# Kernel tuning notes

Hardware: AMD Instinct MI355X
Metric: run time of the kernel (lower is better)

## Reference

```python
import jax, jax.numpy as jnp
import numpy as np

INPUT_SIZE = 1024
HIDDEN_SIZE = 1024
B, L = 32, 2048


def setup_inputs() -> dict:
    key = jax.random.key(0)
    k_h, k_m, k_lw, k_vw, k_vq = jax.random.split(key, 5)
    h = jax.random.normal(k_h, (B, L, INPUT_SIZE), dtype=jnp.float32)
    mask = jax.random.randint(k_m, (B, L), 0, 2).astype(bool)
    # nn.Linear(input+hidden, hidden): weight (hidden, input+hidden), bias (hidden,)
    fan = INPUT_SIZE + HIDDEN_SIZE + HIDDEN_SIZE
    ln_w = jax.random.uniform(k_lw, (HIDDEN_SIZE, INPUT_SIZE + HIDDEN_SIZE),
                              minval=-1.0, maxval=1.0, dtype=jnp.float32) * np.sqrt(6.0 / fan)
    ln_b = jnp.zeros((HIDDEN_SIZE,), dtype=jnp.float32)
    # v: Linear(hidden, 1, bias=False) -> weight (1, hidden); store as (hidden,)
    v_w = jax.random.uniform(k_vw, (HIDDEN_SIZE,), minval=-1.0, maxval=1.0,
                             dtype=jnp.float32) * np.sqrt(6.0 / (HIDDEN_SIZE + 1))
    vq = jax.random.uniform(k_vq, (HIDDEN_SIZE,), dtype=jnp.float32)
    return {"h": h, "mask": mask, "ln_w": ln_w, "ln_b": ln_b, "v_w": v_w, "vq": vq}


def reference(h, mask, ln_w, ln_b, v_w, vq):
    # ln(cat([h, vq], -1)) == h @ W_h^T + vq @ W_vq^T + b  (vq is constant over b,l)
    W_h = ln_w[:, :INPUT_SIZE]          # (H, I)
    W_vq = ln_w[:, INPUT_SIZE:]         # (H, H)
    bias = ln_b + W_vq @ vq             # (H,)
    pre = jnp.einsum('bli,hi->blh', h, W_h) + bias  # (B, L, H)
    s = jnp.tanh(pre) @ v_w             # (B, L)
    s = s - (~mask).astype(s.dtype) * 10000.0
    a = jax.nn.softmax(s, axis=1)       # softmax over seq dim
    r = jnp.einsum('bl,bli->bi', a, h)  # (B, I)
    return r  # dropout omitted (eval mode)
```

## Files before the change

kernel.cpp:

```cpp
#include <hip/hip_runtime.h>
#include <hip/hip_bf16.h>

typedef short  bf16x8s __attribute__((ext_vector_type(8)));
typedef float  f32x4   __attribute__((ext_vector_type(4)));

#define BATCH 32
#define SEQL  2048
#define NROWS (BATCH * SEQL)
#define IN    1024
#define HID   1024

#define BM 128
#define BN 128
#define BK 32

#define WHB_OFF   0u
#define BIAS_OFF  0x200000u
#define SBUF_OFF  0x210000u
#define ABUF_OFF  0x250000u
#define HB_OFF    0x290000u
#define WS_NEED_BF16 ((size_t)HB_OFF + (size_t)NROWS * IN * 2)

__device__ __forceinline__ unsigned int pack2bf(float f0, float f1) {
    unsigned int u0 = __float_as_uint(f0) + 0x8000u;
    unsigned int u1 = __float_as_uint(f1) + 0x8000u;
    return __builtin_amdgcn_perm(u1, u0, 0x07060302u);
}

__device__ __forceinline__ float tanh_fast(float x) {
    float xc = fminf(fmaxf(x, -15.f), 15.f);
    float t  = __builtin_amdgcn_exp2f(xc * 2.8853900817779268f);
    return (t - 1.f) * __builtin_amdgcn_rcpf(t + 1.f);
}

__device__ __forceinline__ void gl2lds16(const void* g, void* l) {
    __builtin_amdgcn_global_load_lds(
        (const __attribute__((address_space(1))) unsigned int*)g,
        (__attribute__((address_space(3))) unsigned int*)l, 16, 0, 0);
}

__device__ __forceinline__ void block_map(int bi, int& rb, int& cb) {
    int xcd  = bi & 7;
    int slot = bi >> 3;
    rb = xcd + 8 * (slot >> 3);
    cb = slot & 7;
}

__global__ __launch_bounds__(256) void prep_kernel(const float* __restrict__ ln_w,
                                                   const float* __restrict__ ln_b,
                                                   const float* __restrict__ vq,
                                                   unsigned short* __restrict__ whb,
                                                   float* __restrict__ bias) {
    const int n = blockIdx.x;
    const int t = threadIdx.x;
    const int wave = t >> 6;
    const int lane = t & 63;
    float4 v = ((const float4*)(ln_w + (size_t)n * 2048))[t];
    uint2 pk;
    pk.x = pack2bf(v.x, v.y);
    pk.y = pack2bf(v.z, v.w);
    *(uint2*)(whb + (size_t)n * 1024 + t * 4) = pk;
    const float* wrow = ln_w + (size_t)n * 2048 + 1024;
    float s = 0.f;
    #pragma unroll
    for (int j = 0; j < 4; ++j) {
        int k = t + j * 256;
        s += wrow[k] * vq[k];
    }
    #pragma unroll
    for (int off = 32; off; off >>= 1) s += __shfl_xor(s, off);
    __shared__ float red[4];
    if (lane == 0) red[wave] = s;
    __syncthreads();
    if (t == 0) bias[n] = ln_b[n] + red[0] + red[1] + red[2] + red[3];
}

__global__ __launch_bounds__(256) void convh_kernel(const float* __restrict__ h,
                                                    unsigned short* __restrict__ hb) {
    size_t idx = ((size_t)blockIdx.x * 256 + threadIdx.x) * 8;
    float4 a = *(const float4*)(h + idx);
    float4 b = *(const float4*)(h + idx + 4);
    uint4 p;
    p.x = pack2bf(a.x, a.y); p.y = pack2bf(a.z, a.w);
    p.z = pack2bf(b.x, b.y); p.w = pack2bf(b.z, b.w);
    *(uint4*)(hb + idx) = p;
}

__global__ __launch_bounds__(256) void gemm_bf16_kernel(const unsigned short* __restrict__ hb,
                                                        const unsigned short* __restrict__ whb,
                                                        const float* __restrict__ bias,
                                                        const float* __restrict__ vw,
                                                        float* __restrict__ s_buf) {
    __shared__ __align__(16) unsigned short As[BM * BK];
    __shared__ __align__(16) unsigned short Bs[BN * BK];

    const int tid = threadIdx.x;
    int rb, cb;
    block_map(blockIdx.x, rb, cb);
    const int wave = tid >> 6;
    const int lane = tid & 63;
    const int quad = lane >> 4;
    const int l15  = lane & 15;
    const int wy   = wave >> 1;
    const int wx   = wave & 1;
    const int row0 = rb * BM;
    const int col0 = cb * BN;

    const int srow = tid >> 2;
    const int sg   = tid & 3;
    const int swz  = (srow >> 1) & 3;
    const unsigned short* gA0 = hb  + (size_t)(row0 + srow) * 1024 + ((sg ^ swz) * 8);
    const unsigned short* gA1 = gA0 + (size_t)64 * 1024;
    const unsigned short* gB0 = whb + (size_t)(col0 + srow) * 1024 + ((sg ^ swz) * 8);
    const unsigned short* gB1 = gB0 + (size_t)64 * 1024;
    unsigned short* lA0 = As + tid * 8;
    unsigned short* lA1 = As + 2048 + tid * 8;
    unsigned short* lB0 = Bs + tid * 8;
    unsigned short* lB1 = Bs + 2048 + tid * 8;

    const unsigned short* rA[4];
    const unsigned short* rB[4];
    #pragma unroll
    for (int i = 0; i < 4; ++i) {
        int ra = wy * 64 + i * 16 + l15;
        rA[i] = As + ra * 32 + ((quad ^ ((ra >> 1) & 3)) * 8);
        int rn = wx * 64 + i * 16 + l15;
        rB[i] = Bs + rn * 32 + ((quad ^ ((rn >> 1) & 3)) * 8);
    }

    f32x4 acc[4][4];
    #pragma unroll
    for (int i = 0; i < 4; ++i)
        #pragma unroll
        for (int j = 0; j < 4; ++j)
            acc[i][j] = (f32x4){0.f, 0.f, 0.f, 0.f};

    for (int k0 = 0; k0 < 1024; k0 += BK) {
        __syncthreads();
        gl2lds16(gA0 + k0, lA0);
        gl2lds16(gA1 + k0, lA1);
        gl2lds16(gB0 + k0, lB0);
        gl2lds16(gB1 + k0, lB1);
        __syncthreads();

        bf16x8s af[4], bfv[4];
        #pragma unroll
        for (int i = 0; i < 4; ++i) af[i]  = *(const bf16x8s*)rA[i];
        #pragma unroll
        for (int i = 0; i < 4; ++i) bfv[i] = *(const bf16x8s*)rB[i];
        #pragma unroll
        for (int mt = 0; mt < 4; ++mt)
            #pragma unroll
            for (int nt = 0; nt < 4; ++nt)
                acc[mt][nt] = __builtin_amdgcn_mfma_f32_16x16x32_bf16(af[mt], bfv[nt], acc[mt][nt], 0, 0, 0);
    }

    const int colb = col0 + wx * 64 + l15;
    float vwv[4], bv[4];
    #pragma unroll
    for (int nt = 0; nt < 4; ++nt) {
        vwv[nt] = vw[colb + nt * 16];
        bv[nt]  = bias[colb + nt * 16];
    }
    const int rowb = row0 + wy * 64 + quad * 4;
    #pragma unroll
    for (int mt = 0; mt < 4; ++mt) {
        #pragma unroll
        for (int r = 0; r < 4; ++r) {
            float p = 0.f;
            #pragma unroll
            for (int nt = 0; nt < 4; ++nt)
                p += tanh_fast(acc[mt][nt][r] + bv[nt]) * vwv[nt];
            p += __shfl_xor(p, 1);
            p += __shfl_xor(p, 2);
            p += __shfl_xor(p, 4);
            p += __shfl_xor(p, 8);
            if (l15 == 0) atomicAdd(&s_buf[rowb + mt * 16 + r], p);
        }
    }
}

__global__ __launch_bounds__(256) void gemm_tanh_kernel(const float* __restrict__ hmat,
                                                        const unsigned short* __restrict__ whb,
                                                        const float* __restrict__ bias,
                                                        const float* __restrict__ vw,
                                                        float* __restrict__ s_buf) {
    __shared__ __align__(16) unsigned short As[BM * BK];
    __shared__ __align__(16) unsigned short Bs[BN * BK];

    const int tid = threadIdx.x;
    int rb, cb;
    block_map(blockIdx.x, rb, cb);
    const int wave = tid >> 6;
    const int lane = tid & 63;
    const int quad = lane >> 4;
    const int l15  = lane & 15;
    const int wy   = wave >> 1;
    const int wx   = wave & 1;
    const int row0 = rb * BM;
    const int col0 = cb * BN;

    const int srow = tid >> 2;
    const int sg   = tid & 3;
    const int swz  = (srow >> 1) & 3;
    const float*          gA0 = hmat + (size_t)(row0 + srow)      * 1024 + sg * 8;
    const float*          gA1 = hmat + (size_t)(row0 + srow + 64) * 1024 + sg * 8;
    const unsigned short* gB0 = whb  + (size_t)(col0 + srow)      * 1024 + ((sg ^ swz) * 8);
    const unsigned short* gB1 = gB0 + (size_t)64 * 1024;
    unsigned short* wA0 = As + srow * 32 + ((sg ^ swz) * 8);
    unsigned short* wA1 = wA0 + 64 * 32;
    unsigned short* lB0 = Bs + tid * 8;
    unsigned short* lB1 = Bs + 2048 + tid * 8;

    const unsigned short* rA[4];
    const unsigned short* rB[4];
    #pragma unroll
    for (int i = 0; i < 4; ++i) {
        int ra = wy * 64 + i * 16 + l15;
        rA[i] = As + ra * 32 + ((quad ^ ((ra >> 1) & 3)) * 8);
        int rn = wx * 64 + i * 16 + l15;
        rB[i] = Bs + rn * 32 + ((quad ^ ((rn >> 1) & 3)) * 8);
    }

    f32x4 acc[4][4];
    #pragma unroll
    for (int i = 0; i < 4; ++i)
        #pragma unroll
        for (int j = 0; j < 4; ++j)
            acc[i][j] = (f32x4){0.f, 0.f, 0.f, 0.f};

    for (int k0 = 0; k0 < 1024; k0 += BK) {
        float4 va0 = *(const float4*)(gA0 + k0);
        float4 va1 = *(const float4*)(gA0 + k0 + 4);
        float4 va2 = *(const float4*)(gA1 + k0);
        float4 va3 = *(const float4*)(gA1 + k0 + 4);

        __syncthreads();
        gl2lds16(gB0 + k0, lB0);
        gl2lds16(gB1 + k0, lB1);

        uint4 pa0, pa1;
        pa0.x = pack2bf(va0.x, va0.y); pa0.y = pack2bf(va0.z, va0.w);
        pa0.z = pack2bf(va1.x, va1.y); pa0.w = pack2bf(va1.z, va1.w);
        pa1.x = pack2bf(va2.x, va2.y); pa1.y = pack2bf(va2.z, va2.w);
        pa1.z = pack2bf(va3.x, va3.y); pa1.w = pack2bf(va3.z, va3.w);
        *(uint4*)wA0 = pa0;
        *(uint4*)wA1 = pa1;

        __syncthreads();

        bf16x8s af[4], bfv[4];
        #pragma unroll
        for (int i = 0; i < 4; ++i) af[i]  = *(const bf16x8s*)rA[i];
        #pragma unroll
        for (int i = 0; i < 4; ++i) bfv[i] = *(const bf16x8s*)rB[i];
        #pragma unroll
        for (int mt = 0; mt < 4; ++mt)
            #pragma unroll
            for (int nt = 0; nt < 4; ++nt)
                acc[mt][nt] = __builtin_amdgcn_mfma_f32_16x16x32_bf16(af[mt], bfv[nt], acc[mt][nt], 0, 0, 0);
    }

    const int colb = col0 + wx * 64 + l15;
    float vwv[4], bv[4];
    #pragma unroll
    for (int nt = 0; nt < 4; ++nt) {
        vwv[nt] = vw[colb + nt * 16];
        bv[nt]  = bias[colb + nt * 16];
    }
    const int rowb = row0 + wy * 64 + quad * 4;
    #pragma unroll
    for (int mt = 0; mt < 4; ++mt) {
        #pragma unroll
        for (int r = 0; r < 4; ++r) {
            float p = 0.f;
            #pragma unroll
            for (int nt = 0; nt < 4; ++nt)
                p += tanh_fast(acc[mt][nt][r] + bv[nt]) * vwv[nt];
            p += __shfl_xor(p, 1);
            p += __shfl_xor(p, 2);
            p += __shfl_xor(p, 4);
            p += __shfl_xor(p, 8);
            if (l15 == 0) atomicAdd(&s_buf[rowb + mt * 16 + r], p);
        }
    }
}

__global__ __launch_bounds__(256) void softmax_kernel(const float* __restrict__ s_buf,
                                                      const int* __restrict__ mask,
                                                      float* __restrict__ a_buf) {
    const int b    = blockIdx.x;
    const int t    = threadIdx.x;
    const int wave = t >> 6;
    const int lane = t & 63;
    __shared__ float redm[4];
    __shared__ float reds[4];
    float sv[8];
    float mx = -3.0e38f;
    #pragma unroll
    for (int j = 0; j < 8; ++j) {
        int l = t + j * 256;
        float v = s_buf[b * 2048 + l];
        if (mask[b * 2048 + l] == 0) v -= 10000.f;
        sv[j] = v;
        mx = fmaxf(mx, v);
    }
    #pragma unroll
    for (int off = 32; off; off >>= 1) mx = fmaxf(mx, __shfl_xor(mx, off));
    if (lane == 0) redm[wave] = mx;
    __syncthreads();
    mx = fmaxf(fmaxf(redm[0], redm[1]), fmaxf(redm[2], redm[3]));
    float sum = 0.f;
    #pragma unroll
    for (int j = 0; j < 8; ++j) {
        sv[j] = __expf(sv[j] - mx);
        sum += sv[j];
    }
    #pragma unroll
    for (int off = 32; off; off >>= 1) sum += __shfl_xor(sum, off);
    if (lane == 0) reds[wave] = sum;
    __syncthreads();
    sum = reds[0] + reds[1] + reds[2] + reds[3];
    float inv = 1.f / sum;
    #pragma unroll
    for (int j = 0; j < 8; ++j)
        a_buf[b * 2048 + t + j * 256] = sv[j] * inv;
}

__global__ __launch_bounds__(256) void r_kernel(const float* __restrict__ hmat,
                                                const float* __restrict__ a_buf,
                                                float* __restrict__ out) {
    const int b  = blockIdx.x >> 5;
    const int lc = blockIdx.x & 31;
    const int t  = threadIdx.x;
    __shared__ float aw[64];
    if (t < 64) aw[t] = a_buf[b * 2048 + lc * 64 + t];
    __syncthreads();
    const float4* hp = (const float4*)hmat + (size_t)(b * 2048 + lc * 64) * 256;
    float ax = 0.f, ay = 0.f, az = 0.f, aq = 0.f;
    #pragma unroll 8
    for (int l = 0; l < 64; ++l) {
        float4 hv = hp[(size_t)l * 256 + t];
        float av = aw[l];
        ax += av * hv.x; ay += av * hv.y; az += av * hv.z; aq += av * hv.w;
    }
    float* op = out + b * 1024 + t * 4;
    atomicAdd(op + 0, ax);
    atomicAdd(op + 1, ay);
    atomicAdd(op + 2, az);
    atomicAdd(op + 3, aq);
}

extern "C" void kernel_launch(void* const* d_in, const int* in_sizes, int n_in,
                              void* d_out, int out_size, void* d_ws, size_t ws_size,
                              hipStream_t stream) {
    const float* h    = (const float*)d_in[0];
    const int*   mask = (const int*)d_in[1];
    const float* ln_w = (const float*)d_in[2];
    const float* ln_b = (const float*)d_in[3];
    const float* v_w  = (const float*)d_in[4];
    const float* vq   = (const float*)d_in[5];
    float* out = (float*)d_out;

    char* ws = (char*)d_ws;
    unsigned short* whb = (unsigned short*)(ws + WHB_OFF);
    float* bias         = (float*)(ws + BIAS_OFF);
    float* s_buf        = (float*)(ws + SBUF_OFF);
    float* a_buf        = (float*)(ws + ABUF_OFF);
    unsigned short* hb  = (unsigned short*)(ws + HB_OFF);

    const bool use_bf16_h = (ws_size >= WS_NEED_BF16);

    hipMemsetAsync(s_buf, 0, NROWS * sizeof(float), stream);
    hipMemsetAsync(d_out, 0, (size_t)out_size * sizeof(float), stream);

    prep_kernel<<<1024, 256, 0, stream>>>(ln_w, ln_b, vq, whb, bias);
    if (use_bf16_h) {
        convh_kernel<<<32768, 256, 0, stream>>>(h, hb);
        gemm_bf16_kernel<<<(NROWS / BM) * (HID / BN), 256, 0, stream>>>(hb, whb, bias, v_w, s_buf);
    } else {
        gemm_tanh_kernel<<<(NROWS / BM) * (HID / BN), 256, 0, stream>>>(h, whb, bias, v_w, s_buf);
    }
    softmax_kernel<<<BATCH, 256, 0, stream>>>(s_buf, mask, a_buf);
    r_kernel<<<BATCH * 32, 256, 0, stream>>>(h, a_buf, out);
}
```

Baseline: 608.5 us.

## Merge prep/convert kernels, deepen GEMM K-step, replace atomics with partials, bf16 r-pass

Fuses the weight prep and h-to-bf16 conversion into one launch and drops the two memsets. Output zeroing moves into the softmax kernel, which also sums 16 per-column-block partial score buffers that replace the atomicAdd reduction. The GEMM loads a 64-wide K slab per barrier pair, halving syncs. The final weighted sum reads the bf16 copy of h instead of fp32, halving that pass's traffic at some precision cost.

```diff
diff --git a/kernel.cpp b/kernel.cpp
--- a/kernel.cpp
+++ b/kernel.cpp
@@ -12,13 +12,12 @@
 
 #define BM 128
 #define BN 128
-#define BK 32
 
 #define WHB_OFF   0u
 #define BIAS_OFF  0x200000u
-#define SBUF_OFF  0x210000u
-#define ABUF_OFF  0x250000u
-#define HB_OFF    0x290000u
+#define SPART_OFF 0x210000u
+#define ABUF_OFF  0x610000u
+#define HB_OFF    0x650000u
 #define WS_NEED_BF16 ((size_t)HB_OFF + (size_t)NROWS * IN * 2)
 
 __device__ __forceinline__ unsigned int pack2bf(float f0, float f1) {
@@ -49,50 +48,52 @@
 __global__ __launch_bounds__(256) void prep_kernel(const float* __restrict__ ln_w,
                                                    const float* __restrict__ ln_b,
                                                    const float* __restrict__ vq,
+                                                   const float* __restrict__ h,
                                                    unsigned short* __restrict__ whb,
-                                                   float* __restrict__ bias) {
-    const int n = blockIdx.x;
-    const int t = threadIdx.x;
-    const int wave = t >> 6;
-    const int lane = t & 63;
-    float4 v = ((const float4*)(ln_w + (size_t)n * 2048))[t];
-    uint2 pk;
-    pk.x = pack2bf(v.x, v.y);
-    pk.y = pack2bf(v.z, v.w);
-    *(uint2*)(whb + (size_t)n * 1024 + t * 4) = pk;
-    const float* wrow = ln_w + (size_t)n * 2048 + 1024;
-    float s = 0.f;
-    #pragma unroll
-    for (int j = 0; j < 4; ++j) {
-        int k = t + j * 256;
-        s += wrow[k] * vq[k];
-    }
-    #pragma unroll
-    for (int off = 32; off; off >>= 1) s += __shfl_xor(s, off);
-    __shared__ float red[4];
-    if (lane == 0) red[wave] = s;
-    __syncthreads();
-    if (t == 0) bias[n] = ln_b[n] + red[0] + red[1] + red[2] + red[3];
-}
-
-__global__ __launch_bounds__(256) void convh_kernel(const float* __restrict__ h,
-                                                    unsigned short* __restrict__ hb) {
-    size_t idx = ((size_t)blockIdx.x * 256 + threadIdx.x) * 8;
-    float4 a = *(const float4*)(h + idx);
-    float4 b = *(const float4*)(h + idx + 4);
-    uint4 p;
-    p.x = pack2bf(a.x, a.y); p.y = pack2bf(a.z, a.w);
-    p.z = pack2bf(b.x, b.y); p.w = pack2bf(b.z, b.w);
-    *(uint4*)(hb + idx) = p;
-}
-
-__global__ __launch_bounds__(256) void gemm_bf16_kernel(const unsigned short* __restrict__ hb,
-                                                        const unsigned short* __restrict__ whb,
-                                                        const float* __restrict__ bias,
-                                                        const float* __restrict__ vw,
-                                                        float* __restrict__ s_buf) {
-    __shared__ __align__(16) unsigned short As[BM * BK];
-    __shared__ __align__(16) unsigned short Bs[BN * BK];
+                                                   float* __restrict__ bias,
+                                                   unsigned short* __restrict__ hb) {
+    const int bi = blockIdx.x;
+    const int t  = threadIdx.x;
+    if (bi < 1024) {
+        const int n = bi;
+        const int wave = t >> 6;
+        const int lane = t & 63;
+        float4 v = ((const float4*)(ln_w + (size_t)n * 2048))[t];
+        uint2 pk;
+        pk.x = pack2bf(v.x, v.y);
+        pk.y = pack2bf(v.z, v.w);
+        *(uint2*)(whb + (size_t)n * 1024 + t * 4) = pk;
+        const float* wrow = ln_w + (size_t)n * 2048 + 1024;
+        float s = 0.f;
+        #pragma unroll
+        for (int j = 0; j < 4; ++j) {
+            int k = t + j * 256;
+            s += wrow[k] * vq[k];
+        }
+        #pragma unroll
+        for (int off = 32; off; off >>= 1) s += __shfl_xor(s, off);
+        __shared__ float red[4];
+        if (lane == 0) red[wave] = s;
+        __syncthreads();
+        if (t == 0) bias[n] = ln_b[n] + red[0] + red[1] + red[2] + red[3];
+    } else {
+        size_t idx = ((size_t)(bi - 1024) * 256 + t) * 8;
+        float4 a = *(const float4*)(h + idx);
+        float4 b = *(const float4*)(h + idx + 4);
+        uint4 p;
+        p.x = pack2bf(a.x, a.y); p.y = pack2bf(a.z, a.w);
+        p.z = pack2bf(b.x, b.y); p.w = pack2bf(b.z, b.w);
+        *(uint4*)(hb + idx) = p;
+    }
+}
+
+__global__ __launch_bounds__(256) void gemm64_kernel(const unsigned short* __restrict__ hb,
+                                                     const unsigned short* __restrict__ whb,
+                                                     const float* __restrict__ bias,
+                                                     const float* __restrict__ vw,
+                                                     float* __restrict__ s_part) {
+    __shared__ __align__(16) unsigned short As[8192];
+    __shared__ __align__(16) unsigned short Bs[8192];
 
     const int tid = threadIdx.x;
     int rb, cb;
@@ -109,14 +110,10 @@
     const int srow = tid >> 2;
     const int sg   = tid & 3;
     const int swz  = (srow >> 1) & 3;
-    const unsigned short* gA0 = hb  + (size_t)(row0 + srow) * 1024 + ((sg ^ swz) * 8);
-    const unsigned short* gA1 = gA0 + (size_t)64 * 1024;
-    const unsigned short* gB0 = whb + (size_t)(col0 + srow) * 1024 + ((sg ^ swz) * 8);
-    const unsigned short* gB1 = gB0 + (size_t)64 * 1024;
-    unsigned short* lA0 = As + tid * 8;
-    unsigned short* lA1 = As + 2048 + tid * 8;
-    unsigned short* lB0 = Bs + tid * 8;
-    unsigned short* lB1 = Bs + 2048 + tid * 8;
+    const unsigned short* gA = hb  + (size_t)(row0 + srow) * 1024 + ((sg ^ swz) * 8);
+    const unsigned short* gB = whb + (size_t)(col0 + srow) * 1024 + ((sg ^ swz) * 8);
+    unsigned short* lA = As + tid * 8;
+    unsigned short* lB = Bs + tid * 8;
 
     const unsigned short* rA[4];
     const unsigned short* rB[4];
@@ -135,24 +132,37 @@
         for (int j = 0; j < 4; ++j)
             acc[i][j] = (f32x4){0.f, 0.f, 0.f, 0.f};
 
-    for (int k0 = 0; k0 < 1024; k0 += BK) {
+    for (int k0 = 0; k0 < 1024; k0 += 64) {
         __syncthreads();
-        gl2lds16(gA0 + k0, lA0);
-        gl2lds16(gA1 + k0, lA1);
-        gl2lds16(gB0 + k0, lB0);
-        gl2lds16(gB1 + k0, lB1);
+        gl2lds16(gA + k0,          lA);
+        gl2lds16(gA + 65536 + k0,  lA + 2048);
+        gl2lds16(gB + k0,          lB);
+        gl2lds16(gB + 65536 + k0,  lB + 2048);
+        gl2lds16(gA + k0 + 32,         lA + 4096);
+        gl2lds16(gA + 65536 + k0 + 32, lA + 6144);
+        gl2lds16(gB + k0 + 32,         lB + 4096);
+        gl2lds16(gB + 65536 + k0 + 32, lB + 6144);
         __syncthreads();
 
-        bf16x8s af[4], bfv[4];
-        #pragma unroll
-        for (int i = 0; i < 4; ++i) af[i]  = *(const bf16x8s*)rA[i];
-        #pragma unroll
-        for (int i = 0; i < 4; ++i) bfv[i] = *(const bf16x8s*)rB[i];
+        bf16x8s af0[4], bf0[4], af1[4], bf1[4];
+        #pragma unroll
+        for (int i = 0; i < 4; ++i) af0[i] = *(const bf16x8s*)rA[i];
+        #pragma unroll
+        for (int i = 0; i < 4; ++i) bf0[i] = *(const bf16x8s*)rB[i];
         #pragma unroll
         for (int mt = 0; mt < 4; ++mt)
             #pragma unroll
             for (int nt = 0; nt < 4; ++nt)
-                acc[mt][nt] = __builtin_amdgcn_mfma_f32_16x16x32_bf16(af[mt], bfv[nt], acc[mt][nt], 0, 0, 0);
+                acc[mt][nt] = __builtin_amdgcn_mfma_f32_16x16x32_bf16(af0[mt], bf0[nt], acc[mt][nt], 0, 0, 0);
+        #pragma unroll
+        for (int i = 0; i < 4; ++i) af1[i] = *(const bf16x8s*)(rA[i] + 4096);
+        #pragma unroll
+        for (int i = 0; i < 4; ++i) bf1[i] = *(const bf16x8s*)(rB[i] + 4096);
+        #pragma unroll
+        for (int mt = 0; mt < 4; ++mt)
+            #pragma unroll
+            for (int nt = 0; nt < 4; ++nt)
+                acc[mt][nt] = __builtin_amdgcn_mfma_f32_16x16x32_bf16(af1[mt], bf1[nt], acc[mt][nt], 0, 0, 0);
     }
 
     const int colb = col0 + wx * 64 + l15;
@@ -163,6 +173,7 @@
         bv[nt]  = bias[colb + nt * 16];
     }
     const int rowb = row0 + wy * 64 + quad * 4;
+    float* sp = s_part + (size_t)(cb * 2 + wx) * NROWS;
     #pragma unroll
     for (int mt = 0; mt < 4; ++mt) {
         #pragma unroll
@@ -175,19 +186,18 @@
             p += __shfl_xor(p, 2);
             p += __shfl_xor(p, 4);
             p += __shfl_xor(p, 8);
-            if (l15 == 0) atomicAdd(&s_buf[rowb + mt * 16 + r], p);
+            if (l15 == 0) sp[rowb + mt * 16 + r] = p;
         }
     }
 }
 
-__global__ __launch_bounds__(256) void gemm_tanh_kernel(const float* __restrict__ hmat,
-                                                        const unsigned short* __restrict__ whb,
-                                                        const float* __restrict__ bias,
-                                                        const float* __restrict__ vw,
-                                                        float* __restrict__ s_buf) {
-    __shared__ __align__(16) unsigned short As[BM * BK];
-    __shared__ __align__(16) unsigned short Bs[BN * BK];
-
+__global__ __launch_bounds__(256) void gemm_f32_kernel(const float* __restrict__ hmat,
+                                                       const unsigned short* __restrict__ whb,
+                                                       const float* __restrict__ bias,
+                                                       const float* __restrict__ vw,
+                                                       float* __restrict__ s_part) {
+    __shared__ __align__(16) unsigned short As[4096];
+    __shared__ __align__(16) unsigned short Bs[4096];
     const int tid = threadIdx.x;
     int rb, cb;
     block_map(blockIdx.x, rb, cb);
@@ -199,19 +209,15 @@
     const int wx   = wave & 1;
     const int row0 = rb * BM;
     const int col0 = cb * BN;
-
     const int srow = tid >> 2;
     const int sg   = tid & 3;
     const int swz  = (srow >> 1) & 3;
     const float*          gA0 = hmat + (size_t)(row0 + srow)      * 1024 + sg * 8;
     const float*          gA1 = hmat + (size_t)(row0 + srow + 64) * 1024 + sg * 8;
     const unsigned short* gB0 = whb  + (size_t)(col0 + srow)      * 1024 + ((sg ^ swz) * 8);
-    const unsigned short* gB1 = gB0 + (size_t)64 * 1024;
     unsigned short* wA0 = As + srow * 32 + ((sg ^ swz) * 8);
     unsigned short* wA1 = wA0 + 64 * 32;
     unsigned short* lB0 = Bs + tid * 8;
-    unsigned short* lB1 = Bs + 2048 + tid * 8;
-
     const unsigned short* rA[4];
     const unsigned short* rB[4];
     #pragma unroll
@@ -221,24 +227,20 @@
         int rn = wx * 64 + i * 16 + l15;
         rB[i] = Bs + rn * 32 + ((quad ^ ((rn >> 1) & 3)) * 8);
     }
-
     f32x4 acc[4][4];
     #pragma unroll
     for (int i = 0; i < 4; ++i)
         #pragma unroll
         for (int j = 0; j < 4; ++j)
             acc[i][j] = (f32x4){0.f, 0.f, 0.f, 0.f};
-
-    for (int k0 = 0; k0 < 1024; k0 += BK) {
+    for (int k0 = 0; k0 < 1024; k0 += 32) {
         float4 va0 = *(const float4*)(gA0 + k0);
         float4 va1 = *(const float4*)(gA0 + k0 + 4);
         float4 va2 = *(const float4*)(gA1 + k0);
         float4 va3 = *(const float4*)(gA1 + k0 + 4);
-
         __syncthreads();
         gl2lds16(gB0 + k0, lB0);
-        gl2lds16(gB1 + k0, lB1);
-
+        gl2lds16(gB0 + 65536 + k0, lB0 + 2048);
         uint4 pa0, pa1;
         pa0.x = pack2bf(va0.x, va0.y); pa0.y = pack2bf(va0.z, va0.w);
         pa0.z = pack2bf(va1.x, va1.y); pa0.w = pack2bf(va1.z, va1.w);
@@ -246,9 +248,7 @@
         pa1.z = pack2bf(va3.x, va3.y); pa1.w = pack2bf(va3.z, va3.w);
         *(uint4*)wA0 = pa0;
         *(uint4*)wA1 = pa1;
-
         __syncthreads();
-
         bf16x8s af[4], bfv[4];
         #pragma unroll
         for (int i = 0; i < 4; ++i) af[i]  = *(const bf16x8s*)rA[i];
@@ -260,7 +260,6 @@
             for (int nt = 0; nt < 4; ++nt)
                 acc[mt][nt] = __builtin_amdgcn_mfma_f32_16x16x32_bf16(af[mt], bfv[nt], acc[mt][nt], 0, 0, 0);
     }
-
     const int colb = col0 + wx * 64 + l15;
     float vwv[4], bv[4];
     #pragma unroll
@@ -269,6 +268,7 @@
         bv[nt]  = bias[colb + nt * 16];
     }
     const int rowb = row0 + wy * 64 + quad * 4;
+    float* sp = s_part + (size_t)(cb * 2 + wx) * NROWS;
     #pragma unroll
     for (int mt = 0; mt < 4; ++mt) {
         #pragma unroll
@@ -281,18 +281,20 @@
             p += __shfl_xor(p, 2);
             p += __shfl_xor(p, 4);
             p += __shfl_xor(p, 8);
-            if (l15 == 0) atomicAdd(&s_buf[rowb + mt * 16 + r], p);
+            if (l15 == 0) sp[rowb + mt * 16 + r] = p;
         }
     }
 }
 
-__global__ __launch_bounds__(256) void softmax_kernel(const float* __restrict__ s_buf,
+__global__ __launch_bounds__(256) void softmax_kernel(const float* __restrict__ s_part,
                                                       const int* __restrict__ mask,
-                                                      float* __restrict__ a_buf) {
+                                                      float* __restrict__ a_buf,
+                                                      float* __restrict__ out) {
     const int b    = blockIdx.x;
     const int t    = threadIdx.x;
     const int wave = t >> 6;
     const int lane = t & 63;
+    ((float4*)(out + b * 1024))[t] = (float4){0.f, 0.f, 0.f, 0.f};
     __shared__ float redm[4];
     __shared__ float reds[4];
     float sv[8];
@@ -300,7 +302,10 @@
     #pragma unroll
     for (int j = 0; j < 8; ++j) {
         int l = t + j * 256;
-        float v = s_buf[b * 2048 + l];
+        float v = 0.f;
+        #pragma unroll
+        for (int c = 0; c < 16; ++c)
+            v += s_part[(size_t)c * NROWS + b * 2048 + l];
         if (mask[b * 2048 + l] == 0) v -= 10000.f;
         sv[j] = v;
         mx = fmaxf(mx, v);
@@ -327,9 +332,36 @@
         a_buf[b * 2048 + t + j * 256] = sv[j] * inv;
 }
 
-__global__ __launch_bounds__(256) void r_kernel(const float* __restrict__ hmat,
-                                                const float* __restrict__ a_buf,
-                                                float* __restrict__ out) {
+__global__ __launch_bounds__(256) void r_bf16_kernel(const unsigned short* __restrict__ hb,
+                                                     const float* __restrict__ a_buf,
+                                                     float* __restrict__ out) {
+    const int b  = blockIdx.x >> 5;
+    const int lc = blockIdx.x & 31;
+    const int t  = threadIdx.x;
+    __shared__ float aw[64];
+    if (t < 64) aw[t] = a_buf[b * 2048 + lc * 64 + t];
+    __syncthreads();
+    const uint2* hp = (const uint2*)(hb + (size_t)(b * 2048 + lc * 64) * 1024) + t;
+    float a0 = 0.f, a1 = 0.f, a2 = 0.f, a3 = 0.f;
+    #pragma unroll 8
+    for (int l = 0; l < 64; ++l) {
+        uint2 v = hp[(size_t)l * 256];
+        float av = aw[l];
+        a0 += av * __uint_as_float(v.x << 16);
+        a1 += av * __uint_as_float(v.x & 0xffff0000u);
+        a2 += av * __uint_as_float(v.y << 16);
+        a3 += av * __uint_as_float(v.y & 0xffff0000u);
+    }
+    float* op = out + b * 1024 + t * 4;
+    atomicAdd(op + 0, a0);
+    atomicAdd(op + 1, a1);
+    atomicAdd(op + 2, a2);
+    atomicAdd(op + 3, a3);
+}
+
+__global__ __launch_bounds__(256) void r_f32_kernel(const float* __restrict__ hmat,
+                                                    const float* __restrict__ a_buf,
+                                                    float* __restrict__ out) {
     const int b  = blockIdx.x >> 5;
     const int lc = blockIdx.x & 31;
     const int t  = threadIdx.x;
@@ -365,22 +397,21 @@
     char* ws = (char*)d_ws;
     unsigned short* whb = (unsigned short*)(ws + WHB_OFF);
     float* bias         = (float*)(ws + BIAS_OFF);
-    float* s_buf        = (float*)(ws + SBUF_OFF);
+    float* s_part       = (float*)(ws + SPART_OFF);
     float* a_buf        = (float*)(ws + ABUF_OFF);
     unsigned short* hb  = (unsigned short*)(ws + HB_OFF);
 
     const bool use_bf16_h = (ws_size >= WS_NEED_BF16);
 
-    hipMemsetAsync(s_buf, 0, NROWS * sizeof(float), stream);
-    hipMemsetAsync(d_out, 0, (size_t)out_size * sizeof(float), stream);
-
-    prep_kernel<<<1024, 256, 0, stream>>>(ln_w, ln_b, vq, whb, bias);
     if (use_bf16_h) {
-        convh_kernel<<<32768, 256, 0, stream>>>(h, hb);
-        gemm_bf16_kernel<<<(NROWS / BM) * (HID / BN), 256, 0, stream>>>(hb, whb, bias, v_w, s_buf);
+        prep_kernel<<<1024 + 32768, 256, 0, stream>>>(ln_w, ln_b, vq, h, whb, bias, hb);
+        gemm64_kernel<<<(NROWS / BM) * (HID / BN), 256, 0, stream>>>(hb, whb, bias, v_w, s_part);
+        softmax_kernel<<<BATCH, 256, 0, stream>>>(s_part, mask, a_buf, out);
+        r_bf16_kernel<<<BATCH * 32, 256, 0, stream>>>(hb, a_buf, out);
     } else {
-        gemm_tanh_kernel<<<(NROWS / BM) * (HID / BN), 256, 0, stream>>>(h, whb, bias, v_w, s_buf);
-    }
-    softmax_kernel<<<BATCH, 256, 0, stream>>>(s_buf, mask, a_buf);
-    r_kernel<<<BATCH * 32, 256, 0, stream>>>(h, a_buf, out);
-}
+        prep_kernel<<<1024, 256, 0, stream>>>(ln_w, ln_b, vq, h, whb, bias, hb);
+        gemm_f32_kernel<<<(NROWS / BM) * (HID / BN), 256, 0, stream>>>(h, whb, bias, v_w, s_part);
+        softmax_kernel<<<BATCH, 256, 0, stream>>>(s_part, mask, a_buf, out);
+        r_f32_kernel<<<BATCH * 32, 256, 0, stream>>>(h, a_buf, out);
+    }
+}
```

After: 601.3 us. About the same (-1.2%).
